# Performance work log

Hardware: AMD Instinct MI355X
Metric: run time of the kernel (lower is better)

Reference implementation:

```python
import jax, jax.numpy as jnp
import numpy as np

G = 8          # grid_size
N = G * G      # 64 nodes
DEG = 17       # neighbors per node for 8x8 sudoku (2x4 boxes)
STEPS = 32
H = 96         # hidden_dim
E = 16         # embed_size
B = 16         # batch


def sudoku_edges():
    # row (7) + col (7) + 2x4 box (7) neighbors, set-union -> 17 per node
    idx = np.arange(N).reshape(G, G)
    nb = []
    for j in range(N):
        r, c = j // G, j % G
        br, bc = (r // 2) * 2, (c // 4) * 4
        s = set(idx[r, :].tolist()) | set(idx[:, c].tolist()) | set(idx[br:br + 2, bc:bc + 4].flatten().tolist())
        s.discard(j)
        nb.append(sorted(s))
    return np.asarray(nb, dtype=np.int32)  # [64, 17]


def setup_inputs() -> dict:
    key = jax.random.key(0)
    ks = jax.random.split(key, 16)
    sc = 0.05
    inp = {
        "x": jax.random.randint(ks[0], (B, G, G), 0, G + 1),            # given digits, 0 = blank
        "target": jax.random.randint(ks[1], (B, G, G), 0, G) + 1,       # solutions in 1..8
        "edges": jnp.asarray(sudoku_edges()),                            # [64, 17] int32
        "digit_emb": jax.random.normal(ks[2], (G + 1, E), jnp.float32) * sc,
        "row_emb": jax.random.normal(ks[3], (G, E), jnp.float32) * sc,
        "col_emb": jax.random.normal(ks[4], (G, E), jnp.float32) * sc,
        "in0_W": jax.random.normal(ks[5], (3 * E, H), jnp.float32) * sc,
        "in0_b": jnp.zeros((H,), jnp.float32),
        "in_Ws": jax.random.normal(ks[6], (3, H, H), jnp.float32) * sc,
        "in_bs": jnp.zeros((3, H), jnp.float32),
        "msg0_W": jax.random.normal(ks[7], (2 * H, H), jnp.float32) * sc,
        "msg0_b": jnp.zeros((H,), jnp.float32),
        "msg_Ws": jax.random.normal(ks[8], (3, H, H), jnp.float32) * sc,
        "msg_bs": jnp.zeros((3, H), jnp.float32),
        "W_ih": jax.random.normal(ks[9], (2 * H, 4 * H), jnp.float32) * sc,
        "W_hh": jax.random.normal(ks[10], (H, 4 * H), jnp.float32) * sc,
        "b_ih": jnp.zeros((4 * H,), jnp.float32),
        "b_hh": jnp.zeros((4 * H,), jnp.float32),
        "pred_W": jax.random.normal(ks[11], (H, G), jnp.float32) * sc,
        "pred_b": jnp.zeros((G,), jnp.float32),
    }
    return inp


def _mlp(z, W0, b0, Ws, bs):
    # Linear -> ReLU -> Linear -> ReLU -> Linear -> ReLU -> Linear (def_MLP)
    z = jax.nn.relu(z @ W0 + b0)
    z = jax.nn.relu(z @ Ws[0] + bs[0])
    z = jax.nn.relu(z @ Ws[1] + bs[1])
    return z @ Ws[2] + bs[2]


def reference(x, target, edges, digit_emb, row_emb, col_emb,
              in0_W, in0_b, in_Ws, in_bs,
              msg0_W, msg0_b, msg_Ws, msg_bs,
              W_ih, W_hh, b_ih, b_hh, pred_W, pred_b):
    bsz = x.shape[0]
    xf = x.reshape(bsz, N)
    tgt = target.reshape(bsz, N) - 1                      # labels 0..7

    de = digit_emb[xf]                                    # [B,64,E]
    re = row_emb[jnp.repeat(jnp.arange(G), G)]            # [64,E]
    ce = col_emb[jnp.tile(jnp.arange(G), G)]              # [64,E]
    feat = jnp.concatenate([de,
                            jnp.broadcast_to(re[None], (bsz, N, E)),
                            jnp.broadcast_to(ce[None], (bsz, N, E))], axis=-1)
    xin = _mlp(feat, in0_W, in0_b, in_Ws, in_bs)          # [B,64,H]

    h0 = jnp.zeros((bsz, N, H), jnp.float32)
    s0 = jnp.zeros((bsz * N, H), jnp.float32)

    def step(carry, _):
        h, s, loss = carry
        # gather-by-edge message passing
        h_edges = h[:, edges]                                             # [B,64,17,H]
        h_self = jnp.broadcast_to(h[:, :, None, :], (bsz, N, DEG, H))
        msg = _mlp(jnp.concatenate([h_edges, h_self], -1),
                   msg0_W, msg0_b, msg_Ws, msg_bs).sum(axis=2)            # [B,64,H]
        # LSTMCell update
        lstm_in = jnp.concatenate([msg, xin], -1).reshape(bsz * N, 2 * H)
        gates = lstm_in @ W_ih + b_ih + h.reshape(bsz * N, H) @ W_hh + b_hh
        i, f, g, o = jnp.split(gates, 4, axis=-1)
        s2 = jax.nn.sigmoid(f) * s + jax.nn.sigmoid(i) * jnp.tanh(g)
        h2 = (jax.nn.sigmoid(o) * jnp.tanh(s2)).reshape(bsz, N, H)
        # per-step prediction / loss / accuracy
        logp = jax.nn.log_softmax(h2 @ pred_W + pred_b, axis=-1)          # [B,64,8]
        pred = jnp.argmax(logp, axis=-1)
        acc = jnp.mean(jnp.all(pred == tgt, axis=1).astype(jnp.float32))
        loss_n = -jnp.sum(jnp.take_along_axis(logp, tgt[..., None], -1)) / (bsz * N)
        return (h2, s2, loss + loss_n), acc

    (h, s, loss), accs = jax.lax.scan(step, (h0, s0, jnp.float32(0.0)), None, length=STEPS)
    loss = loss / STEPS
    final_pred = jnp.argmax(h @ pred_W + pred_b, axis=-1)                 # [B,64]
    return loss, accs, final_pred
```

## Files before the change

### kernel.cpp

```cpp
#include <hip/hip_runtime.h>

#define DEG 17
#define NSTEPS 32
#define HD 96
#define NODES 1024

#define WS_U0     0
#define WS_BAR    196608
#define WS_U1     196864
#define WS_XIN    393472
#define WS_GX     491776
#define WS_LOSSP  884992
#define WS_CNTP   893184

#define Z1    0
#define Z2    7680
#define P3    0
#define PL    0
#define PU    0
#define W1L   15360
#define W2L   24576
#define GXL   33792
#define GATES 35328
#define MSGH  36864
#define S3T   37632
#define H2T   38016
#define SLC   38400
#define MSGB  38784
#define M0B   39072
#define LGT   39168
#define NBRI  39200
#define SMTOT 39280

__global__ void init_kernel(
    const int* __restrict__ x,
    const float* __restrict__ digit_emb,
    const float* __restrict__ row_emb,
    const float* __restrict__ col_emb,
    const float* __restrict__ in0_W,
    const float* __restrict__ in0_b,
    const float* __restrict__ in_Ws,
    const float* __restrict__ in_bs,
    const float* __restrict__ msg0_b,
    float* __restrict__ xin,
    float* __restrict__ u0)
{
  const int node = blockIdx.x;
  const int j = threadIdx.x;
  const int n = node & 63;
  const int r = n >> 3, c = n & 7;
  __shared__ float feat[48];
  __shared__ float za[HD];
  __shared__ float zb[HD];
  if (j < 16)      feat[j] = digit_emb[x[node]*16 + j];
  else if (j < 32) feat[j] = row_emb[r*16 + (j-16)];
  else if (j < 48) feat[j] = col_emb[c*16 + (j-32)];
  u0[node*192 + 96 + j] = msg0_b[j];
  __syncthreads();
  float a = in0_b[j];
  for (int k = 0; k < 48; ++k) a = fmaf(feat[k], in0_W[k*HD + j], a);
  za[j] = fmaxf(a, 0.f);
  __syncthreads();
  a = in_bs[j];
  for (int k = 0; k < HD; ++k) a = fmaf(za[k], in_Ws[k*HD + j], a);
  zb[j] = fmaxf(a, 0.f);
  __syncthreads();
  a = in_bs[HD + j];
  for (int k = 0; k < HD; ++k) a = fmaf(zb[k], in_Ws[9216 + k*HD + j], a);
  za[j] = fmaxf(a, 0.f);
  __syncthreads();
  a = in_bs[2*HD + j];
  for (int k = 0; k < HD; ++k) a = fmaf(za[k], in_Ws[2*9216 + k*HD + j], a);
  xin[node*HD + j] = a;
}

__global__ __launch_bounds__(384) void gx_kernel(
    const float* __restrict__ xin, const float* __restrict__ W_ih,
    const float* __restrict__ b_ih, const float* __restrict__ b_hh,
    float* __restrict__ gx)
{
  __shared__ float xs[4*HD];
  const int tid = threadIdx.x;
  const int base = blockIdx.x * 4;
  {
    const int m = tid / HD, k = tid - m*HD;
    xs[m*HD + k] = xin[(base+m)*HD + k];
  }
  __syncthreads();
  const int j = tid;
  float a0 = b_ih[j] + b_hh[j], a1 = a0, a2 = a0, a3 = a0;
  for (int k = 0; k < HD; ++k) {
    const float w = W_ih[(96+k)*384 + j];
    a0 = fmaf(xs[k], w, a0);
    a1 = fmaf(xs[HD+k], w, a1);
    a2 = fmaf(xs[2*HD+k], w, a2);
    a3 = fmaf(xs[3*HD+k], w, a3);
  }
  gx[(base+0)*384 + j] = a0;
  gx[(base+1)*384 + j] = a1;
  gx[(base+2)*384 + j] = a2;
  gx[(base+3)*384 + j] = a3;
}

__global__ __launch_bounds__(512, 1) void solve_kernel(
    const int* __restrict__ edges,
    const float* __restrict__ msg0_W, const float* __restrict__ msg0_b,
    const float* __restrict__ msg_Ws, const float* __restrict__ msg_bs,
    const float* __restrict__ W_ih, const float* __restrict__ W_hh,
    const float* __restrict__ pred_W, const float* __restrict__ pred_b,
    const int* __restrict__ target,
    const float* __restrict__ gx,
    float* __restrict__ u0, float* __restrict__ u1,
    int* bar,
    float* __restrict__ lossP, int* __restrict__ cntP,
    float* __restrict__ final_pred_out)
{
  __shared__ float sm[SMTOT];

  const int tid = threadIdx.x;
  const int blk = blockIdx.x;
  const int bb = blk & 15;
  const int grp = blk >> 4;
  const int nbase = grp * 4;
  const int base = bb*64 + nbase;

  for (int i = tid*4; i < 9216; i += 2048) {
    *(float4*)&sm[W1L + i] = *(const float4*)&msg_Ws[i];
    *(float4*)&sm[W2L + i] = *(const float4*)&msg_Ws[9216 + i];
  }
  #pragma unroll
  for (int t = 0; t < 3; ++t) {
    const int idx = t*512 + tid;
    sm[GXL + idx] = gx[base*384 + idx];
  }
  if (tid < 288) sm[MSGB + tid] = msg_bs[tid];
  if (tid < 96)  sm[M0B + tid]  = msg0_b[tid];
  if (tid < 80) {
    const int m = tid / 20, r = tid % 20;
    ((int*)&sm[NBRI])[tid] = (r < DEG) ? (bb*64 + edges[(nbase+m)*DEG + r])*192 : -1;
  }
  if (tid < 384) {
    sm[SLC + tid] = 0.f;
    sm[MSGH + 384 + tid] = 0.f;
  }
  __syncthreads();

  const float* uP = u0;
  float*       uN = u1;

  for (int st = 0; st < NSTEPS; ++st) {
    if (tid < 480) {
      const int row = tid % 80;
      const int kh  = tid / 80;
      const int m = row / 20;
      const int k0 = kh * 16;
      const int nb = ((const int*)&sm[NBRI])[row];
      if (nb >= 0) {
        const float* ue = uP + nb + k0;
        const float* us = uP + (base+m)*192 + 96 + k0;
        #pragma unroll
        for (int t = 0; t < 4; ++t) {
          const float4 a = *(const float4*)(ue + 4*t);
          const float4 b = *(const float4*)(us + 4*t);
          sm[Z1 + (k0+4*t+0)*80 + row] = fmaxf(a.x + b.x, 0.f);
          sm[Z1 + (k0+4*t+1)*80 + row] = fmaxf(a.y + b.y, 0.f);
          sm[Z1 + (k0+4*t+2)*80 + row] = fmaxf(a.z + b.z, 0.f);
          sm[Z1 + (k0+4*t+3)*80 + row] = fmaxf(a.w + b.w, 0.f);
        }
      } else {
        #pragma unroll
        for (int t = 0; t < 16; ++t) sm[Z1 + (k0+t)*80 + row] = 0.f;
      }
    } else {
      const int i = tid - 480;
      #pragma unroll
      for (int t = 0; t < 12; ++t) sm[S3T + t*32 + i] = 0.f;
    }
    __syncthreads();

    if (tid < 480) {
      const int jg = tid % 24, dg = tid / 24;
      const int j4 = jg*4, d4 = dg*4;
      float acc[4][4] = {{0.f}};
      #pragma unroll 4
      for (int k = 0; k < 96; ++k) {
        const float4 z = *(const float4*)&sm[Z1 + k*80 + d4];
        const float4 w = *(const float4*)&sm[W1L + k*96 + j4];
        const float ze[4] = {z.x, z.y, z.z, z.w};
        const float we[4] = {w.x, w.y, w.z, w.w};
        #pragma unroll
        for (int dd = 0; dd < 4; ++dd)
          #pragma unroll
          for (int jj = 0; jj < 4; ++jj)
            acc[dd][jj] = fmaf(ze[dd], we[jj], acc[dd][jj]);
      }
      #pragma unroll
      for (int jj = 0; jj < 4; ++jj) {
        const float b1 = sm[MSGB + j4 + jj];
        float4 q;
        q.x = fmaxf(acc[0][jj] + b1, 0.f);
        q.y = fmaxf(acc[1][jj] + b1, 0.f);
        q.z = fmaxf(acc[2][jj] + b1, 0.f);
        q.w = fmaxf(acc[3][jj] + b1, 0.f);
        *(float4*)&sm[Z2 + (j4+jj)*80 + d4] = q;
      }
    }
    __syncthreads();

    if (tid < 480) {
      const int jg = tid % 24, dg = tid / 24;
      const int j4 = jg*4, d4 = dg*4;
      float acc[4][4] = {{0.f}};
      #pragma unroll 4
      for (int k = 0; k < 96; ++k) {
        const float4 z = *(const float4*)&sm[Z2 + k*80 + d4];
        const float4 w = *(const float4*)&sm[W2L + k*96 + j4];
        const float ze[4] = {z.x, z.y, z.z, z.w};
        const float we[4] = {w.x, w.y, w.z, w.w};
        #pragma unroll
        for (int dd = 0; dd < 4; ++dd)
          #pragma unroll
          for (int jj = 0; jj < 4; ++jj)
            acc[dd][jj] = fmaf(ze[dd], we[jj], acc[dd][jj]);
      }
      const int nd = d4 / 20;
      const int r0 = d4 - nd*20;
      #pragma unroll
      for (int jj = 0; jj < 4; ++jj) {
        const float b2 = sm[MSGB + 96 + j4 + jj];
        float p = 0.f;
        #pragma unroll
        for (int dd = 0; dd < 4; ++dd)
          if (r0 + dd < DEG) p += fmaxf(acc[dd][jj] + b2, 0.f);
        atomicAdd(&sm[S3T + (j4+jj)*4 + nd], p);
      }
    }
    __syncthreads();

    if (tid < 384) {
      const int jg = tid % 24, kq = tid / 24;
      const int j4 = jg*4, k0 = kq*6;
      const float* W3 = msg_Ws + 2*9216;
      float acc[4][4] = {{0.f}};
      #pragma unroll
      for (int kk = 0; kk < 6; ++kk) {
        const int k = k0 + kk;
        const float4 sv = *(const float4*)&sm[S3T + k*4];
        const float4 wv = *(const float4*)&W3[k*96 + j4];
        const float se[4] = {sv.x, sv.y, sv.z, sv.w};
        const float we[4] = {wv.x, wv.y, wv.z, wv.w};
        #pragma unroll
        for (int m = 0; m < 4; ++m)
          #pragma unroll
          for (int jj = 0; jj < 4; ++jj)
            acc[m][jj] = fmaf(se[m], we[jj], acc[m][jj]);
      }
      #pragma unroll
      for (int m = 0; m < 4; ++m) {
        float4 q = {acc[m][0], acc[m][1], acc[m][2], acc[m][3]};
        *(float4*)&sm[P3 + (kq*4 + m)*96 + j4] = q;
      }
    }
    __syncthreads();
    if (tid < 384) {
      const int m = tid / 96, j = tid % 96;
      float v = 17.f * sm[MSGB + 192 + j];
      #pragma unroll
      for (int kq = 0; kq < 16; ++kq) v += sm[P3 + (kq*4 + m)*96 + j];
      sm[MSGH + j*4 + m] = v;
    }
    __syncthreads();

    {
      const int jg = tid & 63, kq = tid >> 6;
      const int j6 = jg*6, k0 = kq*24;
      const float* Wb = (k0 < 96) ? (W_ih + (size_t)k0*384) : (W_hh + (size_t)(k0-96)*384);
      float acc[4][6] = {{0.f}};
      #pragma unroll 4
      for (int kk = 0; kk < 24; ++kk) {
        const float4 iv = *(const float4*)&sm[MSGH + (k0+kk)*4];
        const float* wp = Wb + kk*384 + j6;
        const float2 wa = *(const float2*)wp;
        const float2 wb2 = *(const float2*)(wp + 2);
        const float2 wc = *(const float2*)(wp + 4);
        const float ie[4] = {iv.x, iv.y, iv.z, iv.w};
        const float we[6] = {wa.x, wa.y, wb2.x, wb2.y, wc.x, wc.y};
        #pragma unroll
        for (int m = 0; m < 4; ++m)
          #pragma unroll
          for (int jj = 0; jj < 6; ++jj)
            acc[m][jj] = fmaf(ie[m], we[jj], acc[m][jj]);
      }
      #pragma unroll
      for (int m = 0; m < 4; ++m) {
        float2 qa = {acc[m][0], acc[m][1]};
        float2 qb = {acc[m][2], acc[m][3]};
        float2 qc = {acc[m][4], acc[m][5]};
        *(float2*)&sm[PL + (kq*4 + m)*384 + j6]     = qa;
        *(float2*)&sm[PL + (kq*4 + m)*384 + j6 + 2] = qb;
        *(float2*)&sm[PL + (kq*4 + m)*384 + j6 + 4] = qc;
      }
    }
    __syncthreads();
    {
      #pragma unroll
      for (int t = 0; t < 3; ++t) {
        const int idx = t*512 + tid;
        const int m = idx / 384, j = idx - m*384;
        float gv = sm[GXL + idx];
        #pragma unroll
        for (int kq = 0; kq < 8; ++kq) gv += sm[PL + (kq*4 + m)*384 + j];
        sm[GATES + idx] = gv;
      }
    }
    __syncthreads();

    if (tid < 384) {
      const int m = tid / 96, hj = tid - m*96;
      const float gi = sm[GATES + m*384 + hj];
      const float gf = sm[GATES + m*384 + 96 + hj];
      const float gg = sm[GATES + m*384 + 192 + hj];
      const float go = sm[GATES + m*384 + 288 + hj];
      const float sv = sm[SLC + tid];
      const float ig = 1.f/(1.f + expf(-gi));
      const float fg = 1.f/(1.f + expf(-gf));
      const float cg = tanhf(gg);
      const float og = 1.f/(1.f + expf(-go));
      const float s2 = fg*sv + ig*cg;
      const float h2 = og*tanhf(s2);
      sm[SLC + tid] = s2;
      sm[H2T + hj*4 + m] = h2;
      sm[MSGH + (96+hj)*4 + m] = h2;
    }
    __syncthreads();

    {
      const int jg = tid & 31, kq = tid >> 5;
      const int j6 = jg*6, k0 = kq*6;
      const float* Wb = (j6 < 96) ? (msg0_W + j6) : (msg0_W + 9216 + j6 - 96);
      float acc[4][6] = {{0.f}};
      #pragma unroll
      for (int kk = 0; kk < 6; ++kk) {
        const int k = k0 + kk;
        const float4 iv = *(const float4*)&sm[H2T + k*4];
        const float* wp = Wb + k*96;
        const float2 wa = *(const float2*)wp;
        const float2 wb2 = *(const float2*)(wp + 2);
        const float2 wc = *(const float2*)(wp + 4);
        const float ie[4] = {iv.x, iv.y, iv.z, iv.w};
        const float we[6] = {wa.x, wa.y, wb2.x, wb2.y, wc.x, wc.y};
        #pragma unroll
        for (int m = 0; m < 4; ++m)
          #pragma unroll
          for (int jj = 0; jj < 6; ++jj)
            acc[m][jj] = fmaf(ie[m], we[jj], acc[m][jj]);
      }
      #pragma unroll
      for (int m = 0; m < 4; ++m) {
        float2 qa = {acc[m][0], acc[m][1]};
        float2 qb = {acc[m][2], acc[m][3]};
        float2 qc = {acc[m][4], acc[m][5]};
        *(float2*)&sm[PU + (kq*4 + m)*192 + j6]     = qa;
        *(float2*)&sm[PU + (kq*4 + m)*192 + j6 + 2] = qb;
        *(float2*)&sm[PU + (kq*4 + m)*192 + j6 + 4] = qc;
      }
    }
    __syncthreads();
    {
      #pragma unroll
      for (int t = 0; t < 2; ++t) {
        const int idx = t*512 + tid;
        if (idx < 768) {
          const int m = idx / 192, j = idx - m*192;
          float v = (j >= 96) ? sm[M0B + j - 96] : 0.f;
          #pragma unroll
          for (int kq = 0; kq < 16; ++kq) v += sm[PU + (kq*4 + m)*192 + j];
          uN[(base+m)*192 + j] = v;
        }
      }
      if (tid >= 384) {
        const int t2 = tid - 384;
        const int m = t2 >> 5, c = (t2 >> 2) & 7, kq2 = t2 & 3;
        float p = 0.f;
        #pragma unroll
        for (int kk = 0; kk < 24; ++kk) {
          const int k = kq2*24 + kk;
          p = fmaf(sm[H2T + k*4 + m], pred_W[k*8 + c], p);
        }
        p += __shfl_xor(p, 1);
        p += __shfl_xor(p, 2);
        if (kq2 == 0) sm[LGT + m*8 + c] = p + pred_b[c];
      }
    }
    __syncthreads();

    if (tid < 4) {
      const int m = tid;
      const int node = base + m;
      float mx = sm[LGT + m*8];
      int pred = 0;
      #pragma unroll
      for (int c = 1; c < 8; ++c) {
        const float v = sm[LGT + m*8 + c];
        if (v > mx) { mx = v; pred = c; }
      }
      float sum = 0.f;
      #pragma unroll
      for (int c = 0; c < 8; ++c) sum += expf(sm[LGT + m*8 + c] - mx);
      const float lse = mx + logf(sum);
      const int tgt = target[node] - 1;
      sm[LGT + 16 + m] = lse - sm[LGT + m*8 + tgt];
      sm[LGT + 20 + m] = (pred == tgt) ? 1.f : 0.f;
      if (st == NSTEPS-1) final_pred_out[node] = (float)pred;
      if (m == 0) {
        lossP[st*256 + blk] = sm[LGT+16] + sm[LGT+17] + sm[LGT+18] + sm[LGT+19];
        cntP[st*256 + blk] = (int)(sm[LGT+20] + sm[LGT+21] + sm[LGT+22] + sm[LGT+23]);
      }
    }

    if (st < NSTEPS-1) {
      __syncthreads();
      if (tid == 0) {
        __hip_atomic_fetch_add(&bar[bb*16], 1, __ATOMIC_RELEASE, __HIP_MEMORY_SCOPE_AGENT);
        const int want = 16*(st+1);
        while (__hip_atomic_load(&bar[bb*16], __ATOMIC_RELAXED, __HIP_MEMORY_SCOPE_AGENT) < want)
          __builtin_amdgcn_s_sleep(2);
        __threadfence();
      }
      __syncthreads();
      float* tp = (float*)uP; uP = uN; uN = tp;
    }
  }
}

__global__ void finalize_kernel(const float* __restrict__ lossP,
                                const int* __restrict__ cntP,
                                float* __restrict__ out)
{
  __shared__ float sl[32];
  const int tid = threadIdx.x;
  const int st = tid >> 3, q = tid & 7;
  float lsum = 0.f;
  for (int i = 0; i < 32; ++i) lsum += lossP[st*256 + q*32 + i];
  lsum += __shfl_xor(lsum, 1);
  lsum += __shfl_xor(lsum, 2);
  lsum += __shfl_xor(lsum, 4);
  if (q == 0) sl[st] = lsum;
  float okc = 0.f;
  #pragma unroll
  for (int t = 0; t < 2; ++t) {
    const int bbat = q + 8*t;
    int c = 0;
    for (int i = 0; i < 16; ++i) c += cntP[st*256 + i*16 + bbat];
    okc += (c == 64) ? 1.f : 0.f;
  }
  okc += __shfl_xor(okc, 1);
  okc += __shfl_xor(okc, 2);
  okc += __shfl_xor(okc, 4);
  if (q == 0) out[1 + st] = okc / 16.f;
  __syncthreads();
  if (tid == 0) {
    float tot = 0.f;
    for (int i = 0; i < 32; ++i) tot += sl[i];
    out[0] = tot / ((float)NODES * (float)NSTEPS);
  }
}

extern "C" void kernel_launch(void* const* d_in, const int* in_sizes, int n_in,
                              void* d_out, int out_size, void* d_ws, size_t ws_size,
                              hipStream_t stream) {
  const int*   x         = (const int*)  d_in[0];
  const int*   target    = (const int*)  d_in[1];
  const int*   edges     = (const int*)  d_in[2];
  const float* digit_emb = (const float*)d_in[3];
  const float* row_emb   = (const float*)d_in[4];
  const float* col_emb   = (const float*)d_in[5];
  const float* in0_W     = (const float*)d_in[6];
  const float* in0_b     = (const float*)d_in[7];
  const float* in_Ws     = (const float*)d_in[8];
  const float* in_bs     = (const float*)d_in[9];
  const float* msg0_W    = (const float*)d_in[10];
  const float* msg0_b    = (const float*)d_in[11];
  const float* msg_Ws    = (const float*)d_in[12];
  const float* msg_bs    = (const float*)d_in[13];
  const float* W_ih      = (const float*)d_in[14];
  const float* W_hh      = (const float*)d_in[15];
  const float* b_ih      = (const float*)d_in[16];
  const float* b_hh      = (const float*)d_in[17];
  const float* pred_W    = (const float*)d_in[18];
  const float* pred_b    = (const float*)d_in[19];

  float* ws    = (float*)d_ws;
  float* u0    = ws + WS_U0;
  int*   bar   = (int*)(ws + WS_BAR);
  float* u1    = ws + WS_U1;
  float* xin   = ws + WS_XIN;
  float* gxb   = ws + WS_GX;
  float* lossP = ws + WS_LOSSP;
  int*   cntP  = (int*)(ws + WS_CNTP);

  hipMemsetAsync(d_ws, 0, (size_t)(196608 + 256)*sizeof(float), stream);

  init_kernel<<<NODES, HD, 0, stream>>>(x, digit_emb, row_emb, col_emb,
                                        in0_W, in0_b, in_Ws, in_bs,
                                        msg0_b, xin, u0);
  gx_kernel<<<256, 384, 0, stream>>>(xin, W_ih, b_ih, b_hh, gxb);

  float* outp = (float*)d_out;
  solve_kernel<<<256, 512, 0, stream>>>(
      edges, msg0_W, msg0_b, msg_Ws, msg_bs,
      W_ih, W_hh, pred_W, pred_b, target, gxb,
      u0, u1, bar, lossP, cntP, outp + 1 + NSTEPS);

  finalize_kernel<<<1, 256, 0, stream>>>(lossP, cntP, outp);
}
```

Before: 1.097 ms.

## Split solve work across twice as many blocks with two nodes per block

Doubles the persistent solve grid from 256 to 512 blocks, each now handling 2 nodes instead of 4. Shared memory is shrunk by keeping only the first message weight matrix in LDS, reading W2 and the gx precomputation from global, and aliasing scratch buffers. This is meant to spread the per-step serial work over more CUs and shorten each block's critical path, at the cost of more blocks in the per-batch spin barrier and more global/L2 weight reads per step.

```diff
diff --git a/kernel.cpp b/kernel.cpp
--- a/kernel.cpp
+++ b/kernel.cpp
@@ -3,7 +3,6 @@
 #define DEG 17
 #define NSTEPS 32
 #define HD 96
-#define NODES 1024
 
 #define WS_U0     0
 #define WS_BAR    196608
@@ -11,26 +10,21 @@
 #define WS_XIN    393472
 #define WS_GX     491776
 #define WS_LOSSP  884992
-#define WS_CNTP   893184
-
-#define Z1    0
-#define Z2    7680
-#define P3    0
-#define PL    0
-#define PU    0
-#define W1L   15360
-#define W2L   24576
-#define GXL   33792
-#define GATES 35328
-#define MSGH  36864
-#define S3T   37632
-#define H2T   38016
-#define SLC   38400
-#define MSGB  38784
-#define M0B   39072
-#define LGT   39168
-#define NBRI  39200
-#define SMTOT 39280
+#define WS_CNTP   901376
+
+#define W1L    0
+#define MSGB   9216
+#define M0B    9504
+#define MSGH2  9600
+#define GATES2 9984
+#define H2T2   10752
+#define SLC2   10944
+#define LGT    11136
+#define NBRI   11168
+#define S3T    11208
+#define Z1     11592
+#define Z2     15432
+#define SMTOT  19272
 
 __global__ void init_kernel(
     const int* __restrict__ x,
@@ -102,7 +96,7 @@
   gx[(base+3)*384 + j] = a3;
 }
 
-__global__ __launch_bounds__(512, 1) void solve_kernel(
+__global__ __launch_bounds__(512, 4) void solve_kernel(
     const int* __restrict__ edges,
     const float* __restrict__ msg0_W, const float* __restrict__ msg0_b,
     const float* __restrict__ msg_Ws, const float* __restrict__ msg_bs,
@@ -119,29 +113,25 @@
 
   const int tid = threadIdx.x;
   const int blk = blockIdx.x;
-  const int bb = blk & 15;
+  const int bb  = blk & 15;
   const int grp = blk >> 4;
-  const int nbase = grp * 4;
-  const int base = bb*64 + nbase;
-
-  for (int i = tid*4; i < 9216; i += 2048) {
+  const int base = bb*64 + grp*2;
+
+  int* const nbrs = (int*)(sm + NBRI);
+  const float* const W2g = msg_Ws + 9216;
+  const float* const W3g = msg_Ws + 2*9216;
+
+  for (int i = tid*4; i < 9216; i += 2048)
     *(float4*)&sm[W1L + i] = *(const float4*)&msg_Ws[i];
-    *(float4*)&sm[W2L + i] = *(const float4*)&msg_Ws[9216 + i];
-  }
-  #pragma unroll
-  for (int t = 0; t < 3; ++t) {
-    const int idx = t*512 + tid;
-    sm[GXL + idx] = gx[base*384 + idx];
-  }
   if (tid < 288) sm[MSGB + tid] = msg_bs[tid];
   if (tid < 96)  sm[M0B + tid]  = msg0_b[tid];
-  if (tid < 80) {
+  if (tid < 192) {
+    sm[SLC2 + tid] = 0.f;
+    sm[MSGH2 + 192 + tid] = 0.f;
+  }
+  if (tid < 40) {
     const int m = tid / 20, r = tid % 20;
-    ((int*)&sm[NBRI])[tid] = (r < DEG) ? (bb*64 + edges[(nbase+m)*DEG + r])*192 : -1;
-  }
-  if (tid < 384) {
-    sm[SLC + tid] = 0.f;
-    sm[MSGH + 384 + tid] = 0.f;
+    nbrs[tid] = (r < DEG) ? (bb*64 + edges[(grp*2 + m)*DEG + r])*192 : -1;
   }
   __syncthreads();
 
@@ -150,46 +140,46 @@
 
   for (int st = 0; st < NSTEPS; ++st) {
     if (tid < 480) {
-      const int row = tid % 80;
-      const int kh  = tid / 80;
+      const int row = tid % 40;
+      const int kc  = tid / 40;
       const int m = row / 20;
-      const int k0 = kh * 16;
-      const int nb = ((const int*)&sm[NBRI])[row];
+      const int k0 = kc * 8;
+      const int nb = nbrs[row];
       if (nb >= 0) {
         const float* ue = uP + nb + k0;
         const float* us = uP + (base+m)*192 + 96 + k0;
         #pragma unroll
-        for (int t = 0; t < 4; ++t) {
+        for (int t = 0; t < 2; ++t) {
           const float4 a = *(const float4*)(ue + 4*t);
           const float4 b = *(const float4*)(us + 4*t);
-          sm[Z1 + (k0+4*t+0)*80 + row] = fmaxf(a.x + b.x, 0.f);
-          sm[Z1 + (k0+4*t+1)*80 + row] = fmaxf(a.y + b.y, 0.f);
-          sm[Z1 + (k0+4*t+2)*80 + row] = fmaxf(a.z + b.z, 0.f);
-          sm[Z1 + (k0+4*t+3)*80 + row] = fmaxf(a.w + b.w, 0.f);
+          sm[Z1 + (k0+4*t+0)*40 + row] = fmaxf(a.x + b.x, 0.f);
+          sm[Z1 + (k0+4*t+1)*40 + row] = fmaxf(a.y + b.y, 0.f);
+          sm[Z1 + (k0+4*t+2)*40 + row] = fmaxf(a.z + b.z, 0.f);
+          sm[Z1 + (k0+4*t+3)*40 + row] = fmaxf(a.w + b.w, 0.f);
         }
       } else {
         #pragma unroll
-        for (int t = 0; t < 16; ++t) sm[Z1 + (k0+t)*80 + row] = 0.f;
+        for (int t = 0; t < 8; ++t) sm[Z1 + (k0+t)*40 + row] = 0.f;
       }
     } else {
       const int i = tid - 480;
       #pragma unroll
-      for (int t = 0; t < 12; ++t) sm[S3T + t*32 + i] = 0.f;
+      for (int t = 0; t < 12; ++t) sm[S3T + i*12 + t] = 0.f;
     }
     __syncthreads();
 
     if (tid < 480) {
       const int jg = tid % 24, dg = tid / 24;
-      const int j4 = jg*4, d4 = dg*4;
-      float acc[4][4] = {{0.f}};
+      const int j4 = jg*4, d2 = dg*2;
+      float acc[2][4] = {{0.f}};
       #pragma unroll 4
       for (int k = 0; k < 96; ++k) {
-        const float4 z = *(const float4*)&sm[Z1 + k*80 + d4];
+        const float2 z = *(const float2*)&sm[Z1 + k*40 + d2];
         const float4 w = *(const float4*)&sm[W1L + k*96 + j4];
-        const float ze[4] = {z.x, z.y, z.z, z.w};
+        const float ze[2] = {z.x, z.y};
         const float we[4] = {w.x, w.y, w.z, w.w};
         #pragma unroll
-        for (int dd = 0; dd < 4; ++dd)
+        for (int dd = 0; dd < 2; ++dd)
           #pragma unroll
           for (int jj = 0; jj < 4; ++jj)
             acc[dd][jj] = fmaf(ze[dd], we[jj], acc[dd][jj]);
@@ -197,42 +187,40 @@
       #pragma unroll
       for (int jj = 0; jj < 4; ++jj) {
         const float b1 = sm[MSGB + j4 + jj];
-        float4 q;
+        float2 q;
         q.x = fmaxf(acc[0][jj] + b1, 0.f);
         q.y = fmaxf(acc[1][jj] + b1, 0.f);
-        q.z = fmaxf(acc[2][jj] + b1, 0.f);
-        q.w = fmaxf(acc[3][jj] + b1, 0.f);
-        *(float4*)&sm[Z2 + (j4+jj)*80 + d4] = q;
+        *(float2*)&sm[Z2 + (j4+jj)*40 + d2] = q;
       }
     }
     __syncthreads();
 
     if (tid < 480) {
       const int jg = tid % 24, dg = tid / 24;
-      const int j4 = jg*4, d4 = dg*4;
-      float acc[4][4] = {{0.f}};
+      const int j4 = jg*4, d2 = dg*2;
+      float acc[2][4] = {{0.f}};
       #pragma unroll 4
       for (int k = 0; k < 96; ++k) {
-        const float4 z = *(const float4*)&sm[Z2 + k*80 + d4];
-        const float4 w = *(const float4*)&sm[W2L + k*96 + j4];
-        const float ze[4] = {z.x, z.y, z.z, z.w};
+        const float2 z = *(const float2*)&sm[Z2 + k*40 + d2];
+        const float4 w = *(const float4*)&W2g[k*96 + j4];
+        const float ze[2] = {z.x, z.y};
         const float we[4] = {w.x, w.y, w.z, w.w};
         #pragma unroll
-        for (int dd = 0; dd < 4; ++dd)
+        for (int dd = 0; dd < 2; ++dd)
           #pragma unroll
           for (int jj = 0; jj < 4; ++jj)
             acc[dd][jj] = fmaf(ze[dd], we[jj], acc[dd][jj]);
       }
-      const int nd = d4 / 20;
-      const int r0 = d4 - nd*20;
+      const int nd = dg / 10, slot = dg & 1;
+      const int r0 = d2 - nd*20;
       #pragma unroll
       for (int jj = 0; jj < 4; ++jj) {
         const float b2 = sm[MSGB + 96 + j4 + jj];
         float p = 0.f;
         #pragma unroll
-        for (int dd = 0; dd < 4; ++dd)
+        for (int dd = 0; dd < 2; ++dd)
           if (r0 + dd < DEG) p += fmaxf(acc[dd][jj] + b2, 0.f);
-        atomicAdd(&sm[S3T + (j4+jj)*4 + nd], p);
+        atomicAdd(&sm[S3T + (j4+jj)*4 + nd*2 + slot], p);
       }
     }
     __syncthreads();
@@ -240,97 +228,99 @@
     if (tid < 384) {
       const int jg = tid % 24, kq = tid / 24;
       const int j4 = jg*4, k0 = kq*6;
-      const float* W3 = msg_Ws + 2*9216;
-      float acc[4][4] = {{0.f}};
+      float acc[2][4] = {{0.f}};
       #pragma unroll
       for (int kk = 0; kk < 6; ++kk) {
         const int k = k0 + kk;
         const float4 sv = *(const float4*)&sm[S3T + k*4];
-        const float4 wv = *(const float4*)&W3[k*96 + j4];
-        const float se[4] = {sv.x, sv.y, sv.z, sv.w};
+        const float se[2] = {sv.x + sv.y, sv.z + sv.w};
+        const float4 wv = *(const float4*)&W3g[k*96 + j4];
         const float we[4] = {wv.x, wv.y, wv.z, wv.w};
         #pragma unroll
-        for (int m = 0; m < 4; ++m)
+        for (int m = 0; m < 2; ++m)
           #pragma unroll
           for (int jj = 0; jj < 4; ++jj)
             acc[m][jj] = fmaf(se[m], we[jj], acc[m][jj]);
       }
       #pragma unroll
-      for (int m = 0; m < 4; ++m) {
+      for (int m = 0; m < 2; ++m) {
         float4 q = {acc[m][0], acc[m][1], acc[m][2], acc[m][3]};
-        *(float4*)&sm[P3 + (kq*4 + m)*96 + j4] = q;
-      }
-    }
-    __syncthreads();
-    if (tid < 384) {
+        *(float4*)&sm[Z1 + (kq*2 + m)*96 + j4] = q;
+      }
+    }
+    __syncthreads();
+    if (tid < 192) {
       const int m = tid / 96, j = tid % 96;
       float v = 17.f * sm[MSGB + 192 + j];
       #pragma unroll
-      for (int kq = 0; kq < 16; ++kq) v += sm[P3 + (kq*4 + m)*96 + j];
-      sm[MSGH + j*4 + m] = v;
+      for (int kq = 0; kq < 16; ++kq) v += sm[Z1 + (kq*2 + m)*96 + j];
+      sm[MSGH2 + j*2 + m] = v;
     }
     __syncthreads();
 
     {
       const int jg = tid & 63, kq = tid >> 6;
       const int j6 = jg*6, k0 = kq*24;
-      const float* Wb = (k0 < 96) ? (W_ih + (size_t)k0*384) : (W_hh + (size_t)(k0-96)*384);
-      float acc[4][6] = {{0.f}};
+      const float* Wb = (kq < 4) ? (W_ih + (size_t)k0*384 + j6)
+                                 : (W_hh + (size_t)(k0-96)*384 + j6);
+      float acc[2][6] = {{0.f}};
       #pragma unroll 4
       for (int kk = 0; kk < 24; ++kk) {
-        const float4 iv = *(const float4*)&sm[MSGH + (k0+kk)*4];
-        const float* wp = Wb + kk*384 + j6;
+        const float2 iv = *(const float2*)&sm[MSGH2 + (k0+kk)*2];
+        const float* wp = Wb + (size_t)kk*384;
         const float2 wa = *(const float2*)wp;
         const float2 wb2 = *(const float2*)(wp + 2);
         const float2 wc = *(const float2*)(wp + 4);
-        const float ie[4] = {iv.x, iv.y, iv.z, iv.w};
+        const float ie[2] = {iv.x, iv.y};
         const float we[6] = {wa.x, wa.y, wb2.x, wb2.y, wc.x, wc.y};
         #pragma unroll
-        for (int m = 0; m < 4; ++m)
+        for (int m = 0; m < 2; ++m)
           #pragma unroll
           for (int jj = 0; jj < 6; ++jj)
             acc[m][jj] = fmaf(ie[m], we[jj], acc[m][jj]);
       }
       #pragma unroll
-      for (int m = 0; m < 4; ++m) {
+      for (int m = 0; m < 2; ++m) {
         float2 qa = {acc[m][0], acc[m][1]};
         float2 qb = {acc[m][2], acc[m][3]};
         float2 qc = {acc[m][4], acc[m][5]};
-        *(float2*)&sm[PL + (kq*4 + m)*384 + j6]     = qa;
-        *(float2*)&sm[PL + (kq*4 + m)*384 + j6 + 2] = qb;
-        *(float2*)&sm[PL + (kq*4 + m)*384 + j6 + 4] = qc;
+        *(float2*)&sm[Z1 + (kq*2 + m)*384 + j6]     = qa;
+        *(float2*)&sm[Z1 + (kq*2 + m)*384 + j6 + 2] = qb;
+        *(float2*)&sm[Z1 + (kq*2 + m)*384 + j6 + 4] = qc;
       }
     }
     __syncthreads();
     {
       #pragma unroll
-      for (int t = 0; t < 3; ++t) {
+      for (int t = 0; t < 2; ++t) {
         const int idx = t*512 + tid;
-        const int m = idx / 384, j = idx - m*384;
-        float gv = sm[GXL + idx];
-        #pragma unroll
-        for (int kq = 0; kq < 8; ++kq) gv += sm[PL + (kq*4 + m)*384 + j];
-        sm[GATES + idx] = gv;
-      }
-    }
-    __syncthreads();
-
-    if (tid < 384) {
+        if (idx < 768) {
+          const int m = idx / 384, j = idx - m*384;
+          float g = gx[(base+m)*384 + j];
+          #pragma unroll
+          for (int kq = 0; kq < 8; ++kq) g += sm[Z1 + (kq*2 + m)*384 + j];
+          sm[GATES2 + idx] = g;
+        }
+      }
+    }
+    __syncthreads();
+
+    if (tid < 192) {
       const int m = tid / 96, hj = tid - m*96;
-      const float gi = sm[GATES + m*384 + hj];
-      const float gf = sm[GATES + m*384 + 96 + hj];
-      const float gg = sm[GATES + m*384 + 192 + hj];
-      const float go = sm[GATES + m*384 + 288 + hj];
-      const float sv = sm[SLC + tid];
+      const float gi = sm[GATES2 + m*384 + hj];
+      const float gf = sm[GATES2 + m*384 + 96 + hj];
+      const float gg = sm[GATES2 + m*384 + 192 + hj];
+      const float go = sm[GATES2 + m*384 + 288 + hj];
+      const float sv = sm[SLC2 + tid];
       const float ig = 1.f/(1.f + expf(-gi));
       const float fg = 1.f/(1.f + expf(-gf));
       const float cg = tanhf(gg);
       const float og = 1.f/(1.f + expf(-go));
       const float s2 = fg*sv + ig*cg;
       const float h2 = og*tanhf(s2);
-      sm[SLC + tid] = s2;
-      sm[H2T + hj*4 + m] = h2;
-      sm[MSGH + (96+hj)*4 + m] = h2;
+      sm[SLC2 + tid] = s2;
+      sm[H2T2 + hj*2 + m] = h2;
+      sm[MSGH2 + (96+hj)*2 + m] = h2;
     }
     __syncthreads();
 
@@ -338,63 +328,57 @@
       const int jg = tid & 31, kq = tid >> 5;
       const int j6 = jg*6, k0 = kq*6;
       const float* Wb = (j6 < 96) ? (msg0_W + j6) : (msg0_W + 9216 + j6 - 96);
-      float acc[4][6] = {{0.f}};
+      float acc[2][6] = {{0.f}};
       #pragma unroll
       for (int kk = 0; kk < 6; ++kk) {
         const int k = k0 + kk;
-        const float4 iv = *(const float4*)&sm[H2T + k*4];
+        const float2 hv = *(const float2*)&sm[H2T2 + k*2];
         const float* wp = Wb + k*96;
         const float2 wa = *(const float2*)wp;
         const float2 wb2 = *(const float2*)(wp + 2);
         const float2 wc = *(const float2*)(wp + 4);
-        const float ie[4] = {iv.x, iv.y, iv.z, iv.w};
+        const float he[2] = {hv.x, hv.y};
         const float we[6] = {wa.x, wa.y, wb2.x, wb2.y, wc.x, wc.y};
         #pragma unroll
-        for (int m = 0; m < 4; ++m)
+        for (int m = 0; m < 2; ++m)
           #pragma unroll
           for (int jj = 0; jj < 6; ++jj)
-            acc[m][jj] = fmaf(ie[m], we[jj], acc[m][jj]);
-      }
-      #pragma unroll
-      for (int m = 0; m < 4; ++m) {
+            acc[m][jj] = fmaf(he[m], we[jj], acc[m][jj]);
+      }
+      #pragma unroll
+      for (int m = 0; m < 2; ++m) {
         float2 qa = {acc[m][0], acc[m][1]};
         float2 qb = {acc[m][2], acc[m][3]};
         float2 qc = {acc[m][4], acc[m][5]};
-        *(float2*)&sm[PU + (kq*4 + m)*192 + j6]     = qa;
-        *(float2*)&sm[PU + (kq*4 + m)*192 + j6 + 2] = qb;
-        *(float2*)&sm[PU + (kq*4 + m)*192 + j6 + 4] = qc;
-      }
-    }
-    __syncthreads();
-    {
-      #pragma unroll
-      for (int t = 0; t < 2; ++t) {
-        const int idx = t*512 + tid;
-        if (idx < 768) {
-          const int m = idx / 192, j = idx - m*192;
-          float v = (j >= 96) ? sm[M0B + j - 96] : 0.f;
-          #pragma unroll
-          for (int kq = 0; kq < 16; ++kq) v += sm[PU + (kq*4 + m)*192 + j];
-          uN[(base+m)*192 + j] = v;
-        }
-      }
-      if (tid >= 384) {
-        const int t2 = tid - 384;
-        const int m = t2 >> 5, c = (t2 >> 2) & 7, kq2 = t2 & 3;
-        float p = 0.f;
-        #pragma unroll
-        for (int kk = 0; kk < 24; ++kk) {
-          const int k = kq2*24 + kk;
-          p = fmaf(sm[H2T + k*4 + m], pred_W[k*8 + c], p);
-        }
-        p += __shfl_xor(p, 1);
-        p += __shfl_xor(p, 2);
-        if (kq2 == 0) sm[LGT + m*8 + c] = p + pred_b[c];
-      }
-    }
-    __syncthreads();
-
-    if (tid < 4) {
+        *(float2*)&sm[Z1 + (kq*2 + m)*192 + j6]     = qa;
+        *(float2*)&sm[Z1 + (kq*2 + m)*192 + j6 + 2] = qb;
+        *(float2*)&sm[Z1 + (kq*2 + m)*192 + j6 + 4] = qc;
+      }
+    }
+    __syncthreads();
+    if (tid < 384) {
+      const int m = tid / 192, j = tid - m*192;
+      float v = (j >= 96) ? sm[M0B + j - 96] : 0.f;
+      #pragma unroll
+      for (int kq = 0; kq < 16; ++kq) v += sm[Z1 + (kq*2 + m)*192 + j];
+      uN[(base+m)*192 + j] = v;
+    } else {
+      const int t2 = tid - 384;
+      const int m = t2 >> 6, c = (t2 >> 3) & 7, kq2 = t2 & 7;
+      float p = 0.f;
+      #pragma unroll
+      for (int kk = 0; kk < 12; ++kk) {
+        const int k = kq2*12 + kk;
+        p = fmaf(sm[H2T2 + k*2 + m], pred_W[k*8 + c], p);
+      }
+      p += __shfl_xor(p, 1);
+      p += __shfl_xor(p, 2);
+      p += __shfl_xor(p, 4);
+      if (kq2 == 0) sm[LGT + m*8 + c] = p + pred_b[c];
+    }
+    __syncthreads();
+
+    if (tid < 2) {
       const int m = tid;
       const int node = base + m;
       float mx = sm[LGT + m*8];
@@ -410,11 +394,11 @@
       const float lse = mx + logf(sum);
       const int tgt = target[node] - 1;
       sm[LGT + 16 + m] = lse - sm[LGT + m*8 + tgt];
-      sm[LGT + 20 + m] = (pred == tgt) ? 1.f : 0.f;
+      sm[LGT + 18 + m] = (pred == tgt) ? 1.f : 0.f;
       if (st == NSTEPS-1) final_pred_out[node] = (float)pred;
       if (m == 0) {
-        lossP[st*256 + blk] = sm[LGT+16] + sm[LGT+17] + sm[LGT+18] + sm[LGT+19];
-        cntP[st*256 + blk] = (int)(sm[LGT+20] + sm[LGT+21] + sm[LGT+22] + sm[LGT+23]);
+        lossP[st*512 + blk] = sm[LGT+16] + sm[LGT+17];
+        cntP[st*512 + blk] = (int)(sm[LGT+18] + sm[LGT+19]);
       }
     }
 
@@ -422,13 +406,13 @@
       __syncthreads();
       if (tid == 0) {
         __hip_atomic_fetch_add(&bar[bb*16], 1, __ATOMIC_RELEASE, __HIP_MEMORY_SCOPE_AGENT);
-        const int want = 16*(st+1);
+        const int want = 32*(st+1);
         while (__hip_atomic_load(&bar[bb*16], __ATOMIC_RELAXED, __HIP_MEMORY_SCOPE_AGENT) < want)
           __builtin_amdgcn_s_sleep(2);
         __threadfence();
       }
       __syncthreads();
-      float* tp = (float*)uP; uP = uN; uN = tp;
+      const float* tp = uP; uP = uN; uN = (float*)tp;
     }
   }
 }
@@ -441,7 +425,7 @@
   const int tid = threadIdx.x;
   const int st = tid >> 3, q = tid & 7;
   float lsum = 0.f;
-  for (int i = 0; i < 32; ++i) lsum += lossP[st*256 + q*32 + i];
+  for (int i = 0; i < 64; ++i) lsum += lossP[st*512 + q*64 + i];
   lsum += __shfl_xor(lsum, 1);
   lsum += __shfl_xor(lsum, 2);
   lsum += __shfl_xor(lsum, 4);
@@ -451,7 +435,7 @@
   for (int t = 0; t < 2; ++t) {
     const int bbat = q + 8*t;
     int c = 0;
-    for (int i = 0; i < 16; ++i) c += cntP[st*256 + i*16 + bbat];
+    for (int i = 0; i < 32; ++i) c += cntP[st*512 + i*16 + bbat];
     okc += (c == 64) ? 1.f : 0.f;
   }
   okc += __shfl_xor(okc, 1);
@@ -462,7 +446,7 @@
   if (tid == 0) {
     float tot = 0.f;
     for (int i = 0; i < 32; ++i) tot += sl[i];
-    out[0] = tot / ((float)NODES * (float)NSTEPS);
+    out[0] = tot / (1024.f * (float)NSTEPS);
   }
 }
 
@@ -501,13 +485,13 @@
 
   hipMemsetAsync(d_ws, 0, (size_t)(196608 + 256)*sizeof(float), stream);
 
-  init_kernel<<<NODES, HD, 0, stream>>>(x, digit_emb, row_emb, col_emb,
-                                        in0_W, in0_b, in_Ws, in_bs,
-                                        msg0_b, xin, u0);
+  init_kernel<<<1024, HD, 0, stream>>>(x, digit_emb, row_emb, col_emb,
+                                       in0_W, in0_b, in_Ws, in_bs,
+                                       msg0_b, xin, u0);
   gx_kernel<<<256, 384, 0, stream>>>(xin, W_ih, b_ih, b_hh, gxb);
 
   float* outp = (float*)d_out;
-  solve_kernel<<<256, 512, 0, stream>>>(
+  solve_kernel<<<512, 512, 0, stream>>>(
       edges, msg0_W, msg0_b, msg_Ws, msg_bs,
       W_ih, W_hh, pred_W, pred_b, target, gxb,
       u0, u1, bar, lossP, cntP, outp + 1 + NSTEPS);
```

After: 2.542 ms. 2.32x slower.
